# Kernel optimization log

Measured on AMD Instinct MI355X. Metric: run time of the kernel, lower is better.

## Reference

```python
import jax, jax.numpy as jnp
import numpy as np

EPS = 1e-12  # matches torch F.normalize eps
TEMPERATURE = 1.0
LAMBDA = 0.8


def _l2norm(x):
    n = jnp.sqrt(jnp.sum(x * x, axis=-1, keepdims=True))
    return x / jnp.maximum(n, EPS)


def setup_inputs() -> dict:
    key = jax.random.key(0)
    feats = jax.random.normal(key, (4, 4096, 512), dtype=jnp.float32)
    return {"feats": feats, "node": 8}


def reference(feats, node):
    f = _l2norm(feats)                                   # [B,N,D]
    scores = jnp.einsum('bnd,bmd->bnm', f, f) / TEMPERATURE  # [B,N,N]
    vals, idx = jax.lax.top_k(scores, node)              # [B,N,k]
    B, N, _ = scores.shape
    bi = jnp.arange(B)[:, None, None]
    ni = jnp.arange(N)[None, :, None]
    sparse = jnp.full_like(scores, -jnp.inf).at[bi, ni, idx].set(vals)
    w = jax.nn.softmax(sparse, axis=-1)                  # zeros outside top-k
    feats_att = jnp.einsum('bnm,bmd->bnd', w, f)
    feats_gam = f * LAMBDA + feats_att * (1.0 - LAMBDA)
    return _l2norm(feats_gam)
```

## Files before the change

### kernel.cpp

```cpp
#include <hip/hip_runtime.h>
#include <stdint.h>

#define NROWS 4096
#define NDIM  512
#define TOPT  8
#define NLIST 16
#define NCAND 128
#define NRESC 12
#define KSEL  8

typedef __attribute__((ext_vector_type(8))) short short8;
typedef __attribute__((ext_vector_type(4))) float f32x4;

__device__ __forceinline__ unsigned short f2bf(float x) {
  unsigned int u = __float_as_uint(x);
  return (unsigned short)((u + 0x7fffu + ((u >> 16) & 1u)) >> 16);
}

__device__ __forceinline__ void gl_lds16(const void* g, void* l) {
  void* gnc = (void*)g;
  __builtin_amdgcn_global_load_lds(
      (__attribute__((address_space(1))) void*)gnc,
      (__attribute__((address_space(3))) void*)l, 16, 0, 0);
}

__device__ __forceinline__ void ins8(unsigned int (&tv)[TOPT], unsigned int k) {
#pragma unroll
  for (int j = 0; j < TOPT; ++j) {
    const unsigned int nt = tv[j] > k ? tv[j] : k;
    k = tv[j] > k ? k : tv[j];
    tv[j] = nt;
  }
}

__global__ __launch_bounds__(256) void k_norm(const float* __restrict__ in,
                                              float* __restrict__ fout,
                                              unsigned short* __restrict__ fbf) {
  const int row = blockIdx.x * 4 + (threadIdx.x >> 6);
  const int l = threadIdx.x & 63;
  const float4* src = reinterpret_cast<const float4*>(in + (size_t)row * NDIM);
  float4 a = src[l * 2], b = src[l * 2 + 1];
  float ss = a.x * a.x + a.y * a.y + a.z * a.z + a.w * a.w +
             b.x * b.x + b.y * b.y + b.z * b.z + b.w * b.w;
#pragma unroll
  for (int off = 32; off; off >>= 1) ss += __shfl_xor(ss, off, 64);
  const float inv = 1.0f / fmaxf(sqrtf(ss), 1e-12f);
  a.x *= inv; a.y *= inv; a.z *= inv; a.w *= inv;
  b.x *= inv; b.y *= inv; b.z *= inv; b.w *= inv;
  float4* dst = reinterpret_cast<float4*>(fout + (size_t)row * NDIM);
  dst[l * 2] = a; dst[l * 2 + 1] = b;
  uint4 ub;
  ub.x = (unsigned)f2bf(a.x) | ((unsigned)f2bf(a.y) << 16);
  ub.y = (unsigned)f2bf(a.z) | ((unsigned)f2bf(a.w) << 16);
  ub.z = (unsigned)f2bf(b.x) | ((unsigned)f2bf(b.y) << 16);
  ub.w = (unsigned)f2bf(b.z) | ((unsigned)f2bf(b.w) << 16);
  reinterpret_cast<uint4*>(fbf + (size_t)row * NDIM)[l] = ub;
}

__global__ __launch_bounds__(512, 4) void k_coarse(const unsigned short* __restrict__ fbf,
                                                   unsigned int* __restrict__ keys) {
  __shared__ alignas(16) union {
    struct { unsigned short A[128 * 64]; unsigned short B[128 * 64]; } st;
    unsigned short S[128 * 128];
  } sh;

  const int tid = threadIdx.x;
  const int w = tid >> 6, l = tid & 63;

  const int lin = blockIdx.x;
  const int xcd = lin & 7;
  const int slot = lin >> 3;
  const int xq = xcd * 4 + (slot & 3);
  const int ym = (slot >> 2) & 7;
  const int zb = slot >> 5;

  const int q0 = xq * 128;
  const int m0 = ym * 512;
  const int bbase = zb * NROWS;

  const int qh = w >> 2, mq = w & 3;
  const int r = tid >> 2, sub = tid & 3;
  const int rx = r & 31;

  const int lrow = (l >> 3);
  const int lkg  = ((l & 7) ^ lrow) * 8;

  unsigned int tv[TOPT];
#pragma unroll
  for (int j = 0; j < TOPT; ++j) tv[j] = 0u;

  const f32x4 vzero = {0.f, 0.f, 0.f, 0.f};

  for (int mt = 0; mt < 4; ++mt) {
    const int mbase = m0 + mt * 128;
    f32x4 acc[4][2];
#pragma unroll
    for (int i = 0; i < 4; ++i)
#pragma unroll
      for (int j = 0; j < 2; ++j) acc[i][j] = vzero;

    for (int kt = 0; kt < 8; ++kt) {
      const int kk = kt * 64;
#pragma unroll
      for (int t = 0; t < 2; ++t) {
        const int sa = w * 2 + t;
        const int srow = sa * 8 + lrow;
        gl_lds16(fbf + ((size_t)(bbase + q0 + srow) << 9) + kk + lkg,
                 &sh.st.A[sa * 512]);
        gl_lds16(fbf + ((size_t)(bbase + mbase + srow) << 9) + kk + lkg,
                 &sh.st.B[sa * 512]);
      }
      __syncthreads();
#pragma unroll
      for (int ks = 0; ks < 2; ++ks) {
        short8 av[4], bv[2];
        const int kgrp = ks * 4 + (l >> 4);
#pragma unroll
        for (int i = 0; i < 4; ++i) {
          const int row = qh * 64 + i * 16 + (l & 15);
          av[i] = *(const short8*)&sh.st.A[row * 64 + (kgrp ^ (l & 7)) * 8];
        }
#pragma unroll
        for (int j = 0; j < 2; ++j) {
          const int row = mq * 32 + j * 16 + (l & 15);
          bv[j] = *(const short8*)&sh.st.B[row * 64 + (kgrp ^ (l & 7)) * 8];
        }
#pragma unroll
        for (int i = 0; i < 4; ++i)
#pragma unroll
          for (int j = 0; j < 2; ++j)
            acc[i][j] = __builtin_amdgcn_mfma_f32_16x16x32_bf16(av[i], bv[j], acc[i][j], 0, 0, 0);
      }
      __syncthreads();
    }

#pragma unroll
    for (int i = 0; i < 4; ++i) {
      const int qb_ = qh * 64 + i * 16 + (l >> 4) * 4;
#pragma unroll
      for (int j = 0; j < 2; ++j) {
        const int mc = mq * 32 + j * 16 + (l & 15);
#pragma unroll
        for (int rr = 0; rr < 4; ++rr) {
          const int q = qb_ + rr;
          unsigned int uu = __float_as_uint(acc[i][j][rr]);
          uu ^= (unsigned int)(((int)uu) >> 31) | 0x80000000u;
          const int pg = ((mc >> 2) ^ (q & 31));
          sh.S[q * 128 + pg * 4 + (mc & 3)] = (unsigned short)(uu >> 16);
        }
      }
    }
    __syncthreads();

    {
      const int invb0 = 4095 - (mbase + sub * 32);
#pragma unroll 4
      for (int cg = 0; cg < 8; ++cg) {
        const int pg = (sub * 8 + cg) ^ rx;
        const ushort4 s4 = *(const ushort4*)&sh.S[r * 128 + pg * 4];
        const unsigned int invb = (unsigned int)(invb0 - cg * 4);
        const unsigned int k0 = ((unsigned int)s4.x << 16) | invb;
        const unsigned int k1 = ((unsigned int)s4.y << 16) | (invb - 1);
        const unsigned int k2 = ((unsigned int)s4.z << 16) | (invb - 2);
        const unsigned int k3 = ((unsigned int)s4.w << 16) | (invb - 3);
        if (k0 > tv[TOPT - 1]) ins8(tv, k0);
        if (k1 > tv[TOPT - 1]) ins8(tv, k1);
        if (k2 > tv[TOPT - 1]) ins8(tv, k2);
        if (k3 > tv[TOPT - 1]) ins8(tv, k3);
      }
    }
    __syncthreads();
  }

  unsigned int ov[TOPT];
#pragma unroll
  for (int j = 0; j < TOPT; ++j) ov[j] = __shfl_xor(tv[j], 1, 64);
  unsigned int mg[TOPT];
#pragma unroll
  for (int j = 0; j < TOPT; ++j) {
    const unsigned int o = ov[TOPT - 1 - j];
    mg[j] = tv[j] > o ? tv[j] : o;
  }

  if ((sub & 1) == 0) {
    const int list = ym * 2 + (sub >> 1);
    unsigned int* dst = keys + (((size_t)(bbase + q0 + r)) * NLIST + list) * TOPT;
    reinterpret_cast<uint4*>(dst)[0] = make_uint4(mg[0], mg[1], mg[2], mg[3]);
    reinterpret_cast<uint4*>(dst)[1] = make_uint4(mg[4], mg[5], mg[6], mg[7]);
  }
}

__global__ __launch_bounds__(256) void k_final(const float* __restrict__ f,
                                               const unsigned int* __restrict__ keys,
                                               float* __restrict__ out) {
  const int lin = blockIdx.x;
  const int xcd = lin & 7;
  const int slot = lin >> 3;
  const int b = xcd >> 1;
  const int n = ((xcd & 1) * 512 + slot) * 4 + (threadIdx.x >> 6);
  const int qg = b * NROWS + n;
  const int l = threadIdx.x & 63;

  const uint2 kk = reinterpret_cast<const uint2*>(keys + (size_t)qg * NCAND)[l];
  unsigned int ka = kk.x, kb = kk.y;

  int si[NRESC];
#pragma unroll
  for (int rr = 0; rr < NRESC; ++rr) {
    unsigned int v = ka > kb ? ka : kb;
#pragma unroll
    for (int off = 32; off; off >>= 1) {
      const unsigned int o = __shfl_xor(v, off, 64);
      v = o > v ? o : v;
    }
    si[rr] = __builtin_amdgcn_readfirstlane(4095 - (int)(v & 4095u));
    if (ka == v) ka = 0u;
    if (kb == v) kb = 0u;
  }

  const float* __restrict__ fb = f + (size_t)b * NROWS * NDIM;
  const float* frow = fb + (size_t)n * NDIM;
  float selfv[8];
#pragma unroll
  for (int c = 0; c < 8; ++c) selfv[c] = frow[c * 64 + l];

  double ex[NRESC];
#pragma unroll
  for (int rr = 0; rr < NRESC; ++rr) {
    const float* g = fb + (size_t)si[rr] * NDIM;
    double s = 0.0;
#pragma unroll
    for (int c = 0; c < 8; ++c) s += (double)selfv[c] * (double)g[c * 64 + l];
#pragma unroll
    for (int off = 32; off; off >>= 1) s += __shfl_xor(s, off, 64);
    ex[rr] = s;
  }

  unsigned mask = 0;
  double wex[KSEL]; int wi[KSEL];
#pragma unroll
  for (int rr = 0; rr < KSEL; ++rr) {
    double mv = -1.0e300; int midx = 0x7fffffff; int mslot = 0;
#pragma unroll
    for (int j = 0; j < NRESC; ++j) {
      const bool avail = ((mask >> j) & 1u) == 0u;
      if (avail && (ex[j] > mv || (ex[j] == mv && si[j] < midx))) {
        mv = ex[j]; midx = si[j]; mslot = j;
      }
    }
    mask |= 1u << mslot;
    wex[rr] = mv; wi[rr] = midx;
  }

  float w8[KSEL];
  const float mx = (float)wex[0];
  float wsum = 0.f;
#pragma unroll
  for (int rr = 0; rr < KSEL; ++rr) { w8[rr] = expf((float)wex[rr] - mx); wsum += w8[rr]; }
  const float cs = 0.2f / wsum;

  float acc[8];
#pragma unroll
  for (int c = 0; c < 8; ++c) acc[c] = 0.8f * selfv[c];
#pragma unroll
  for (int rr = 0; rr < KSEL; ++rr) {
    const float* g = fb + (size_t)wi[rr] * NDIM;
    const float wr = cs * w8[rr];
#pragma unroll
    for (int c = 0; c < 8; ++c) acc[c] = fmaf(wr, g[c * 64 + l], acc[c]);
  }

  float ss = 0.f;
#pragma unroll
  for (int c = 0; c < 8; ++c) ss += acc[c] * acc[c];
#pragma unroll
  for (int off = 32; off; off >>= 1) ss += __shfl_xor(ss, off, 64);
  const float inv = 1.0f / fmaxf(sqrtf(ss), 1e-12f);
  float* orow = out + (size_t)qg * NDIM;
#pragma unroll
  for (int c = 0; c < 8; ++c) orow[c * 64 + l] = acc[c] * inv;
}

extern "C" void kernel_launch(void* const* d_in, const int* in_sizes, int n_in,
                              void* d_out, int out_size, void* d_ws, size_t ws_size,
                              hipStream_t stream) {
  (void)in_sizes; (void)n_in; (void)out_size; (void)ws_size;
  const float* feats = (const float*)d_in[0];
  char* ws = (char*)d_ws;
  float*          fnorm = (float*)(ws);
  unsigned short* fbf   = (unsigned short*)(ws + 33554432);
  unsigned int*   keys  = (unsigned int*)(ws + 50331648);
  float* out = (float*)d_out;

  k_norm<<<dim3(4096), dim3(256), 0, stream>>>(feats, fnorm, fbf);
  k_coarse<<<dim3(1024), dim3(512), 0, stream>>>(fbf, keys);
  k_final<<<dim3(4096), dim3(256), 0, stream>>>(fnorm, keys, out);
}
```

Baseline: 279.3 us.

## Double-buffer global-to-LDS tile loads in coarse similarity GEMM

Splits shared memory into two A/B staging buffers so the next K-slice, or the first slice of the next M tile, is fetched with global_load_lds while MFMAs run on the current buffer. The score scratch area now overlays the second buffer instead of a union. Full __syncthreads are replaced by explicit waitcnt plus s_barrier, and s_setprio is raised around the MFMA block. Shared memory per block doubles to 64KB, which may cut resident blocks per CU below the launch-bounds target.

```diff
diff --git a/kernel.cpp b/kernel.cpp
--- a/kernel.cpp
+++ b/kernel.cpp
@@ -59,10 +59,7 @@
 
 __global__ __launch_bounds__(512, 4) void k_coarse(const unsigned short* __restrict__ fbf,
                                                    unsigned int* __restrict__ keys) {
-  __shared__ alignas(16) union {
-    struct { unsigned short A[128 * 64]; unsigned short B[128 * 64]; } st;
-    unsigned short S[128 * 128];
-  } sh;
+  __shared__ alignas(16) unsigned short shmem[32768];
 
   const int tid = threadIdx.x;
   const int w = tid >> 6, l = tid & 63;
@@ -85,11 +82,30 @@
   const int lrow = (l >> 3);
   const int lkg  = ((l & 7) ^ lrow) * 8;
 
+  unsigned short* const S = shmem + 16384;
+
+  auto stage = [&](int mb, int kk, int par) {
+#pragma unroll
+    for (int t = 0; t < 2; ++t) {
+      const int sa = w * 2 + t;
+      const int srow = sa * 8 + lrow;
+      gl_lds16(fbf + ((size_t)(bbase + q0 + srow) << 9) + kk + lkg,
+               shmem + par * 16384 + sa * 512);
+      gl_lds16(fbf + ((size_t)(bbase + mb + srow) << 9) + kk + lkg,
+               shmem + par * 16384 + 8192 + sa * 512);
+    }
+  };
+
   unsigned int tv[TOPT];
 #pragma unroll
   for (int j = 0; j < TOPT; ++j) tv[j] = 0u;
 
   const f32x4 vzero = {0.f, 0.f, 0.f, 0.f};
+
+  stage(m0, 0, 0);
+  asm volatile("s_waitcnt vmcnt(0)" ::: "memory");
+  __builtin_amdgcn_sched_barrier(0);
+  __builtin_amdgcn_s_barrier();
 
   for (int mt = 0; mt < 4; ++mt) {
     const int mbase = m0 + mt * 128;
@@ -99,18 +115,15 @@
 #pragma unroll
       for (int j = 0; j < 2; ++j) acc[i][j] = vzero;
 
+#pragma unroll
     for (int kt = 0; kt < 8; ++kt) {
-      const int kk = kt * 64;
-#pragma unroll
-      for (int t = 0; t < 2; ++t) {
-        const int sa = w * 2 + t;
-        const int srow = sa * 8 + lrow;
-        gl_lds16(fbf + ((size_t)(bbase + q0 + srow) << 9) + kk + lkg,
-                 &sh.st.A[sa * 512]);
-        gl_lds16(fbf + ((size_t)(bbase + mbase + srow) << 9) + kk + lkg,
-                 &sh.st.B[sa * 512]);
-      }
-      __syncthreads();
+      if (kt < 7) {
+        stage(mbase, (kt + 1) * 64, (kt + 1) & 1);
+      } else if (mt < 3) {
+        stage(mbase + 128, 0, 0);
+      }
+      const unsigned short* Ab = shmem + (kt & 1) * 16384;
+      const unsigned short* Bb = Ab + 8192;
 #pragma unroll
       for (int ks = 0; ks < 2; ++ks) {
         short8 av[4], bv[2];
@@ -118,20 +131,29 @@
 #pragma unroll
         for (int i = 0; i < 4; ++i) {
           const int row = qh * 64 + i * 16 + (l & 15);
-          av[i] = *(const short8*)&sh.st.A[row * 64 + (kgrp ^ (l & 7)) * 8];
+          av[i] = *(const short8*)&Ab[row * 64 + (kgrp ^ (l & 7)) * 8];
         }
 #pragma unroll
         for (int j = 0; j < 2; ++j) {
           const int row = mq * 32 + j * 16 + (l & 15);
-          bv[j] = *(const short8*)&sh.st.B[row * 64 + (kgrp ^ (l & 7)) * 8];
+          bv[j] = *(const short8*)&Bb[row * 64 + (kgrp ^ (l & 7)) * 8];
         }
+        asm volatile("s_waitcnt lgkmcnt(0)" ::: "memory");
+        __builtin_amdgcn_sched_barrier(0);
+        __builtin_amdgcn_s_setprio(1);
 #pragma unroll
         for (int i = 0; i < 4; ++i)
 #pragma unroll
           for (int j = 0; j < 2; ++j)
             acc[i][j] = __builtin_amdgcn_mfma_f32_16x16x32_bf16(av[i], bv[j], acc[i][j], 0, 0, 0);
-      }
-      __syncthreads();
+        __builtin_amdgcn_s_setprio(0);
+      }
+      __builtin_amdgcn_sched_barrier(0);
+      if (kt < 7) {
+        asm volatile("s_waitcnt vmcnt(0)" ::: "memory");
+        __builtin_amdgcn_sched_barrier(0);
+      }
+      __builtin_amdgcn_s_barrier();
     }
 
 #pragma unroll
@@ -146,18 +168,20 @@
           unsigned int uu = __float_as_uint(acc[i][j][rr]);
           uu ^= (unsigned int)(((int)uu) >> 31) | 0x80000000u;
           const int pg = ((mc >> 2) ^ (q & 31));
-          sh.S[q * 128 + pg * 4 + (mc & 3)] = (unsigned short)(uu >> 16);
+          S[q * 128 + pg * 4 + (mc & 3)] = (unsigned short)(uu >> 16);
         }
       }
     }
-    __syncthreads();
+    asm volatile("s_waitcnt lgkmcnt(0)" ::: "memory");
+    __builtin_amdgcn_sched_barrier(0);
+    __builtin_amdgcn_s_barrier();
 
     {
       const int invb0 = 4095 - (mbase + sub * 32);
 #pragma unroll 4
       for (int cg = 0; cg < 8; ++cg) {
         const int pg = (sub * 8 + cg) ^ rx;
-        const ushort4 s4 = *(const ushort4*)&sh.S[r * 128 + pg * 4];
+        const ushort4 s4 = *(const ushort4*)&S[r * 128 + pg * 4];
         const unsigned int invb = (unsigned int)(invb0 - cg * 4);
         const unsigned int k0 = ((unsigned int)s4.x << 16) | invb;
         const unsigned int k1 = ((unsigned int)s4.y << 16) | (invb - 1);
@@ -169,7 +193,9 @@
         if (k3 > tv[TOPT - 1]) ins8(tv, k3);
       }
     }
-    __syncthreads();
+    asm volatile("s_waitcnt vmcnt(0) lgkmcnt(0)" ::: "memory");
+    __builtin_amdgcn_sched_barrier(0);
+    __builtin_amdgcn_s_barrier();
   }
 
   unsigned int ov[TOPT];
```

Measured after the change: 281.7 us. About the same (+0.9%).

## Split each final-stage query row across two waves with shared-memory reduction

Applied to the files above, without the earlier changes.

The final rescoring kernel previously gave each query row to a single wave, which computed all 12 fp64 candidate dot products, selected the top 8 by repeated argmax, and gathered them. Now each row uses a 128-thread block of two waves. Each wave handles half the candidate dot products and half the weighted gather, exchanging scores and partial accumulators through LDS. Selection becomes a branch-free rank count instead of sequential argmax. The goal is to shorten the serial dependency chain per row and raise parallelism, at the cost of two block barriers, duplicated key decoding in both waves, and four times as many blocks.

```diff
diff --git a/kernel.cpp b/kernel.cpp
--- a/kernel.cpp
+++ b/kernel.cpp
@@ -190,15 +190,19 @@
   }
 }
 
-__global__ __launch_bounds__(256) void k_final(const float* __restrict__ f,
+__global__ __launch_bounds__(128) void k_final(const float* __restrict__ f,
                                                const unsigned int* __restrict__ keys,
                                                float* __restrict__ out) {
+  __shared__ double sh_ex[NRESC];
+  __shared__ float sh_acc[8 * 64];
+
   const int lin = blockIdx.x;
   const int xcd = lin & 7;
   const int slot = lin >> 3;
   const int b = xcd >> 1;
-  const int n = ((xcd & 1) * 512 + slot) * 4 + (threadIdx.x >> 6);
+  const int n = (xcd & 1) * 2048 + slot;
   const int qg = b * NROWS + n;
+  const int w = threadIdx.x >> 6;
   const int l = threadIdx.x & 63;
 
   const uint2 kk = reinterpret_cast<const uint2*>(keys + (size_t)qg * NCAND)[l];
@@ -224,61 +228,84 @@
 #pragma unroll
   for (int c = 0; c < 8; ++c) selfv[c] = frow[c * 64 + l];
 
-  double ex[NRESC];
-#pragma unroll
-  for (int rr = 0; rr < NRESC; ++rr) {
+#pragma unroll
+  for (int j = 0; j < 6; ++j) {
+    const int rr = j * 2 + w;
     const float* g = fb + (size_t)si[rr] * NDIM;
     double s = 0.0;
 #pragma unroll
     for (int c = 0; c < 8; ++c) s += (double)selfv[c] * (double)g[c * 64 + l];
 #pragma unroll
     for (int off = 32; off; off >>= 1) s += __shfl_xor(s, off, 64);
-    ex[rr] = s;
-  }
-
-  unsigned mask = 0;
-  double wex[KSEL]; int wi[KSEL];
-#pragma unroll
-  for (int rr = 0; rr < KSEL; ++rr) {
-    double mv = -1.0e300; int midx = 0x7fffffff; int mslot = 0;
-#pragma unroll
-    for (int j = 0; j < NRESC; ++j) {
-      const bool avail = ((mask >> j) & 1u) == 0u;
-      if (avail && (ex[j] > mv || (ex[j] == mv && si[j] < midx))) {
-        mv = ex[j]; midx = si[j]; mslot = j;
-      }
-    }
-    mask |= 1u << mslot;
-    wex[rr] = mv; wi[rr] = midx;
-  }
-
-  float w8[KSEL];
-  const float mx = (float)wex[0];
+    if (l == 0) sh_ex[rr] = s;
+  }
+  __syncthreads();
+
+  double ex[NRESC];
+#pragma unroll
+  for (int j = 0; j < NRESC; ++j) ex[j] = sh_ex[j];
+
+  int rank[NRESC];
+#pragma unroll
+  for (int j = 0; j < NRESC; ++j) {
+    int rk = 0;
+#pragma unroll
+    for (int a = 0; a < NRESC; ++a) {
+      if (a != j) {
+        const bool beats = (ex[a] > ex[j]) || (ex[a] == ex[j] && si[a] < si[j]);
+        rk += beats ? 1 : 0;
+      }
+    }
+    rank[j] = rk;
+  }
+  double mxd = ex[0];
+#pragma unroll
+  for (int j = 1; j < NRESC; ++j) mxd = ex[j] > mxd ? ex[j] : mxd;
+
+  const float mxf = (float)mxd;
+  float wj[NRESC];
   float wsum = 0.f;
 #pragma unroll
-  for (int rr = 0; rr < KSEL; ++rr) { w8[rr] = expf((float)wex[rr] - mx); wsum += w8[rr]; }
+  for (int j = 0; j < NRESC; ++j) {
+    const float e = expf((float)ex[j] - mxf);
+    wj[j] = (rank[j] < KSEL) ? e : 0.f;
+    wsum += wj[j];
+  }
   const float cs = 0.2f / wsum;
 
   float acc[8];
 #pragma unroll
-  for (int c = 0; c < 8; ++c) acc[c] = 0.8f * selfv[c];
-#pragma unroll
-  for (int rr = 0; rr < KSEL; ++rr) {
-    const float* g = fb + (size_t)wi[rr] * NDIM;
-    const float wr = cs * w8[rr];
-#pragma unroll
-    for (int c = 0; c < 8; ++c) acc[c] = fmaf(wr, g[c * 64 + l], acc[c]);
-  }
-
-  float ss = 0.f;
-#pragma unroll
-  for (int c = 0; c < 8; ++c) ss += acc[c] * acc[c];
-#pragma unroll
-  for (int off = 32; off; off >>= 1) ss += __shfl_xor(ss, off, 64);
-  const float inv = 1.0f / fmaxf(sqrtf(ss), 1e-12f);
-  float* orow = out + (size_t)qg * NDIM;
-#pragma unroll
-  for (int c = 0; c < 8; ++c) orow[c * 64 + l] = acc[c] * inv;
+  for (int c = 0; c < 8; ++c) acc[c] = (w == 0) ? 0.8f * selfv[c] : 0.f;
+#pragma unroll
+  for (int j = 0; j < 6; ++j) {
+    const int rr = j * 2 + w;
+    if (rank[rr] < KSEL) {
+      const float* g = fb + (size_t)si[rr] * NDIM;
+      const float wr = cs * wj[rr];
+#pragma unroll
+      for (int c = 0; c < 8; ++c) acc[c] = fmaf(wr, g[c * 64 + l], acc[c]);
+    }
+  }
+
+  if (w == 1) {
+#pragma unroll
+    for (int c = 0; c < 8; ++c) sh_acc[c * 64 + l] = acc[c];
+  }
+  __syncthreads();
+  if (w == 0) {
+    float ss = 0.f;
+#pragma unroll
+    for (int c = 0; c < 8; ++c) {
+      acc[c] += sh_acc[c * 64 + l];
+      ss += acc[c] * acc[c];
+    }
+#pragma unroll
+    for (int off = 32; off; off >>= 1) ss += __shfl_xor(ss, off, 64);
+    const float inv = 1.0f / fmaxf(sqrtf(ss), 1e-12f);
+    float* orow = out + (size_t)qg * NDIM;
+#pragma unroll
+    for (int c = 0; c < 8; ++c) orow[c * 64 + l] = acc[c] * inv;
+  }
 }
 
 extern "C" void kernel_launch(void* const* d_in, const int* in_sizes, int n_in,
@@ -294,5 +321,5 @@
 
   k_norm<<<dim3(4096), dim3(256), 0, stream>>>(feats, fnorm, fbf);
   k_coarse<<<dim3(1024), dim3(512), 0, stream>>>(fbf, keys);
-  k_final<<<dim3(4096), dim3(256), 0, stream>>>(fnorm, keys, out);
-}
+  k_final<<<dim3(16384), dim3(128), 0, stream>>>(fnorm, keys, out);
+}
```

Result: slower. 418.4 us (+49.8%).
